# Kernel optimization log

Measured on AMD Instinct MI355X. Metric: run time of the kernel, lower is better.

## Reference

```python
import jax, jax.numpy as jnp
import numpy as np

B, N, C, H, MLP = 4, 1024, 768, 6, 2304  # num_heads = C // 128
D = C // H  # head dim = 128


def setup_inputs() -> dict:
    key = jax.random.key(0)
    ks = iter(jax.random.split(key, 64))
    def nrm(shape, s=0.02):
        return jax.random.normal(next(ks), shape, jnp.float32) * s
    inp = {}
    for nm in ("queries", "change_emb", "imageA_emb", "imageB_emb", "pe"):
        inp[nm] = jax.random.normal(next(ks), (B, N, C), jnp.float32)
    # three Attention modules: self-attn (1), change->ABC cross (2), imageAB->change cross (3)
    for i in (1, 2, 3):
        for p in ("q", "k", "v", "o"):
            inp[f"w{p}{i}"] = nrm((C, C))       # stored [in, out]; y = x @ W + b
            inp[f"b{p}{i}"] = jnp.zeros((C,), jnp.float32)
    for i in (1, 2, 3):
        inp[f"ln{i}_w"] = jnp.ones((C,), jnp.float32)
        inp[f"ln{i}_b"] = jnp.zeros((C,), jnp.float32)
    inp["mlp_w1"] = nrm((C, MLP)); inp["mlp_b1"] = jnp.zeros((MLP,), jnp.float32)
    inp["mlp_w2"] = nrm((MLP, C)); inp["mlp_b2"] = jnp.zeros((C,), jnp.float32)
    inp["flag_a"] = nrm((C,)); inp["flag_b"] = nrm((C,)); inp["flag_c"] = nrm((C,))
    return inp


def _ln(x, w, b, eps=1e-5):
    m = jnp.mean(x, -1, keepdims=True)
    v = jnp.var(x, -1, keepdims=True)
    return (x - m) * jax.lax.rsqrt(v + eps) * w + b


def _mha(q, k, v, wq, bq, wk, bk, wv, bv, wo, bo):
    b, nq, _ = q.shape
    qh = (q @ wq + bq).reshape(b, nq, H, D)
    kh = (k @ wk + bk).reshape(b, k.shape[1], H, D)
    vh = (v @ wv + bv).reshape(b, v.shape[1], H, D)
    scores = jnp.einsum('bqhd,bkhd->bhqk', qh, kh) / np.float32(np.sqrt(D))
    attn = jax.nn.softmax(scores, axis=-1)
    out = jnp.einsum('bhqk,bkhd->bqhd', attn, vh).reshape(b, nq, H * D)
    return out @ wo + bo


def reference(queries, change_emb, imageA_emb, imageB_emb, pe,
              wq1, bq1, wk1, bk1, wv1, bv1, wo1, bo1,
              wq2, bq2, wk2, bk2, wv2, bv2, wo2, bo2,
              wq3, bq3, wk3, bk3, wv3, bv3, wo3, bo3,
              ln1_w, ln1_b, ln2_w, ln2_b, ln3_w, ln3_b,
              mlp_w1, mlp_b1, mlp_w2, mlp_b2,
              flag_a, flag_b, flag_c):
    # --- self attention on change queries (skip_first_layer_add=False) ---
    q0 = queries + change_emb
    a = _mha(q0 + pe, q0 + pe, q0, wq1, bq1, wk1, bk1, wv1, bv1, wo1, bo1)
    q1 = _ln(q0 + a, ln1_w, ln1_b)
    # --- cross attention: change -> [imageA, imageB, change] ---
    qf = q1 + pe + flag_c
    k2 = jnp.concatenate((imageA_emb + pe + flag_a,
                          imageB_emb + pe + flag_b,
                          q1 + pe + flag_c), axis=1)
    v2 = jnp.concatenate((imageA_emb, imageB_emb, q1), axis=1)
    a = _mha(qf, k2, v2, wq2, bq2, wk2, bk2, wv2, bv2, wo2, bo2)
    q2 = _ln(q1 + a, ln2_w, ln2_b)
    # --- MLP (exact GELU, as nn.GELU default) ---
    mlp_out = jax.nn.gelu(q2 @ mlp_w1 + mlp_b1, approximate=False) @ mlp_w2 + mlp_b2
    q3 = _ln(q2 + mlp_out, ln3_w, ln3_b)
    change_out = q3
    # --- cross attention: [imageA; imageB] -> [image; change], batched along dim 0 ---
    qa = imageA_emb + pe + flag_a
    qb = imageB_emb + pe + flag_b
    ka = jnp.concatenate((imageA_emb + pe + flag_a, q3 + pe + flag_c), axis=1)
    kb = jnp.concatenate((imageB_emb + pe + flag_b, q3 + pe + flag_c), axis=1)
    va = jnp.concatenate((imageA_emb, q3), axis=1)
    vb = jnp.concatenate((imageB_emb, q3), axis=1)
    q = jnp.concatenate((qa, qb), axis=0)   # [2B, N, C]
    k = jnp.concatenate((ka, kb), axis=0)   # [2B, 2N, C]
    v = jnp.concatenate((va, vb), axis=0)
    a = _mha(q, k, v, wq3, bq3, wk3, bk3, wv3, bv3, wo3, bo3)
    q = q + a
    image_A_refined, image_B_refined = jnp.split(q, 2, axis=0)
    return (image_A_refined, image_B_refined, change_out)
```

## Files before the change

### kernel.cpp

```cpp
#include <hip/hip_runtime.h>
#include <hip/hip_bf16.h>
#include <math.h>

typedef short bf16x8 __attribute__((ext_vector_type(8)));
typedef float f32x4 __attribute__((ext_vector_type(4)));
using bf16_t = __hip_bfloat16;

#define DEV static __device__ __forceinline__

DEV unsigned short f2bu(float x) {
  bf16_t h = __float2bfloat16(x);
  unsigned short u;
  __builtin_memcpy(&u, &h, 2);
  return u;
}
DEV void st4(bf16_t* p, float a, float b, float c, float d) {
  ushort4 u;
  u.x = f2bu(a); u.y = f2bu(b); u.z = f2bu(c); u.w = f2bu(d);
  *reinterpret_cast<ushort4*>(p) = u;
}

DEV void async_copy16(const bf16_t* g, bf16_t* lds) {
  __builtin_amdgcn_global_load_lds(
      (const __attribute__((address_space(1))) unsigned int*)g,
      (__attribute__((address_space(3))) unsigned int*)lds, 16, 0, 0);
}

struct WPack {
  const float* s[12];
  bf16_t* d[12];
  float scale0;
};

__global__ __launch_bounds__(256) void k_wt12(WPack pk) {
  __shared__ float tile[32][33];
  int z = blockIdx.z;
  const float* W = pk.s[z];
  bf16_t* WT = pk.d[z];
  float scale = (z == 0) ? pk.scale0 : 1.0f;
  int i0 = blockIdx.x * 32;
  int o0 = blockIdx.y * 32;
  int tx = threadIdx.x & 31, ty = threadIdx.x >> 5;
  for (int r = ty; r < 32; r += 8)
    tile[r][tx] = W[(size_t)(i0 + r) * 768 + (o0 + tx)];
  __syncthreads();
  for (int r = ty; r < 32; r += 8)
    WT[(size_t)(o0 + r) * 768 + (i0 + tx)] = __float2bfloat16(tile[tx][r] * scale);
}

__global__ __launch_bounds__(256) void k_wt(const float* __restrict__ W, bf16_t* __restrict__ WT,
                                            int in_dim, int out_dim) {
  __shared__ float tile[32][33];
  int i0 = blockIdx.x * 32;
  int o0 = blockIdx.y * 32;
  int tx = threadIdx.x & 31, ty = threadIdx.x >> 5;
  for (int r = ty; r < 32; r += 8)
    tile[r][tx] = W[(size_t)(i0 + r) * out_dim + (o0 + tx)];
  __syncthreads();
  for (int r = ty; r < 32; r += 8)
    WT[(size_t)(o0 + r) * in_dim + (i0 + tx)] = __float2bfloat16(tile[tx][r]);
}

__global__ __launch_bounds__(256) void k_bqk(const float* __restrict__ bq, const float* __restrict__ bk,
                                             float* __restrict__ out, float qa) {
  int i = blockIdx.x * 256 + threadIdx.x;
  if (i < 768) out[i] = bq[i] * qa;
  else if (i < 1536) out[i] = bk[i - 768];
}

__global__ __launch_bounds__(256) void k_prep1(const float4* __restrict__ q, const float4* __restrict__ ce,
                                               const float4* __restrict__ pe,
                                               bf16_t* __restrict__ qpe_b, bf16_t* __restrict__ q0_b, int n4) {
  int i = blockIdx.x * 256 + threadIdx.x;
  if (i >= n4) return;
  float4 a = q[i], b = ce[i], p = pe[i];
  float sx = a.x + b.x, sy = a.y + b.y, sz = a.z + b.z, sw = a.w + b.w;
  st4(q0_b + 4 * (size_t)i, sx, sy, sz, sw);
  st4(qpe_b + 4 * (size_t)i, sx + p.x, sy + p.y, sz + p.z, sw + p.w);
}

__global__ __launch_bounds__(256) void k_addpe(const float* __restrict__ x, const float* __restrict__ pe,
                                               const float* __restrict__ flag, bf16_t* __restrict__ out) {
  int idx = blockIdx.x * 256 + threadIdx.x;
  int c = (idx % 192) * 4;
  size_t tok = (size_t)idx * 4;
  float4 xv = *(const float4*)(x + tok);
  float4 p = *(const float4*)(pe + tok);
  float4 f = *(const float4*)(flag + c);
  st4(out + tok, xv.x + p.x + f.x, xv.y + p.y + f.y, xv.z + p.z + f.z, xv.w + p.w + f.w);
}

__global__ __launch_bounds__(256) void k_buildqq(const float* __restrict__ imA, const float* __restrict__ imB,
                                                 const float* __restrict__ pe, const float* __restrict__ fa,
                                                 const float* __restrict__ fb, bf16_t* __restrict__ qq) {
  int idx = blockIdx.x * 256 + threadIdx.x;
  int c4 = idx % 192; int rem = idx / 192;
  int n = rem & 1023; int bb = rem >> 10;
  int b = bb & 3, isB = bb >> 2;
  int c = c4 * 4;
  size_t tok = (size_t)(b * 1024 + n) * 768 + c;
  float4 s = *(const float4*)((isB ? imB : imA) + tok);
  float4 p = *(const float4*)(pe + tok);
  float4 f = *(const float4*)((isB ? fb : fa) + c);
  st4(qq + (size_t)rem * 768 + c, s.x + p.x + f.x, s.y + p.y + f.y, s.z + p.z + f.z, s.w + p.w + f.w);
}

__global__ __launch_bounds__(256) void k_build2b(const float* __restrict__ q1,
    const float* __restrict__ imA, const float* __restrict__ imB, const float* __restrict__ pe,
    const float* __restrict__ fa, const float* __restrict__ fb, const float* __restrict__ fc,
    bf16_t* __restrict__ k2, bf16_t* __restrict__ v2, int b0) {
  int idx = blockIdx.x * 256 + threadIdx.x;
  int c4 = idx % 192; int rem = idx / 192;
  int bi = rem / 3072; int r3 = rem - bi * 3072;
  int seg = r3 >> 10; int n = r3 & 1023;
  int b = b0 + bi;
  int c = c4 * 4;
  size_t tok = (size_t)(b * 1024 + n) * 768 + c;
  float4 p = *(const float4*)(pe + tok);
  const float* srcp; const float* flg;
  if (seg == 0)      { srcp = imA + tok; flg = fa; }
  else if (seg == 1) { srcp = imB + tok; flg = fb; }
  else               { srcp = q1 + tok; flg = fc; }
  float4 s = *(const float4*)srcp;
  float4 f = *(const float4*)(flg + c);
  size_t o = (size_t)idx * 4;
  st4(v2 + o, s.x, s.y, s.z, s.w);
  st4(k2 + o, s.x + p.x + f.x, s.y + p.y + f.y, s.z + p.z + f.z, s.w + p.w + f.w);
}

__global__ __launch_bounds__(256) void k_build3b(const float* __restrict__ q3,
    const float* __restrict__ imA, const float* __restrict__ imB, const float* __restrict__ pe,
    const float* __restrict__ fa, const float* __restrict__ fb, const float* __restrict__ fc,
    bf16_t* __restrict__ k3, bf16_t* __restrict__ v3, int bb0) {
  int idx = blockIdx.x * 256 + threadIdx.x;
  int c4 = idx % 192; int rem = idx / 192;
  int bi = rem >> 11; int r2 = rem & 2047;
  int seg = r2 >> 10; int n = r2 & 1023;
  int bb = bb0 + bi;
  int b = bb & 3; int isB = bb >> 2;
  int c = c4 * 4;
  size_t tok = (size_t)(b * 1024 + n) * 768 + c;
  float4 p = *(const float4*)(pe + tok);
  const float* srcp; const float* flg;
  if (seg == 0) { srcp = (isB ? imB : imA) + tok; flg = isB ? fb : fa; }
  else          { srcp = q3 + tok; flg = fc; }
  float4 s = *(const float4*)srcp;
  float4 f = *(const float4*)(flg + c);
  size_t o = (size_t)idx * 4;
  st4(v3 + o, s.x, s.y, s.z, s.w);
  st4(k3 + o, s.x + p.x + f.x, s.y + p.y + f.y, s.z + p.z + f.z, s.w + p.w + f.w);
}

__global__ __launch_bounds__(256, 3) void k_flash(
    const bf16_t* __restrict__ Q, const bf16_t* __restrict__ K,
    const bf16_t* __restrict__ Vt, bf16_t* __restrict__ O,
    int Nk, int H, int ldq, int ldk, long qStrideB, long kStrideB, long oStrideB) {
  const int z = blockIdx.y; const int b = z / H, h = z % H;
  const bf16_t* Qb = Q + (size_t)b * qStrideB + h * 128;
  const bf16_t* Kb = K + (size_t)b * kStrideB + h * 128;
  const bf16_t* Vb = Vt + (size_t)z * 128 * (size_t)Nk;
  bf16_t* Ob = O + (size_t)b * oStrideB + h * 128;
  const int q0 = blockIdx.x * 64;
  const int tid = threadIdx.x, lane = tid & 63, w = tid >> 6;
  const int g = lane >> 4, c = lane & 15;

  __shared__ bf16_t Ks[64][136];
  __shared__ bf16_t Vs[128][72];
  __shared__ bf16_t Ps[64][72];

  bf16x8 qf[4];
#pragma unroll
  for (int kk = 0; kk < 4; kk++)
    qf[kk] = *reinterpret_cast<const bf16x8*>(
        &Qb[(size_t)(q0 + w * 16 + c) * ldq + kk * 32 + g * 8]);

  f32x4 oa[8];
  float m[4], l[4];
#pragma unroll
  for (int d = 0; d < 8; d++) { f32x4 zz = {0.f, 0.f, 0.f, 0.f}; oa[d] = zz; }
#pragma unroll
  for (int r = 0; r < 4; r++) { m[r] = -1.0e30f; l[r] = 0.f; }

  const int kr_ = tid >> 4, kc_ = (tid & 15) * 8;
  const int vr_ = tid >> 3, vc_ = (tid & 7) * 8;

  const int nt = Nk >> 6;
  for (int t = 0; t < nt; ++t) {
    const int k0 = t << 6;
#pragma unroll
    for (int p = 0; p < 4; p++)
      *reinterpret_cast<uint4*>(&Ks[p * 16 + kr_][kc_]) =
          *reinterpret_cast<const uint4*>(&Kb[(size_t)(k0 + p * 16 + kr_) * ldk + kc_]);
#pragma unroll
    for (int p = 0; p < 4; p++)
      *reinterpret_cast<uint4*>(&Vs[p * 32 + vr_][vc_]) =
          *reinterpret_cast<const uint4*>(&Vb[(size_t)(p * 32 + vr_) * Nk + k0 + vc_]);
    __syncthreads();

    f32x4 s[4];
#pragma unroll
    for (int j = 0; j < 4; j++) { f32x4 zz = {0.f, 0.f, 0.f, 0.f}; s[j] = zz; }
    __builtin_amdgcn_s_setprio(1);
#pragma unroll
    for (int kk = 0; kk < 4; kk++)
#pragma unroll
      for (int j = 0; j < 4; j++) {
        bf16x8 kf = *reinterpret_cast<const bf16x8*>(&Ks[j * 16 + c][kk * 32 + g * 8]);
        s[j] = __builtin_amdgcn_mfma_f32_16x16x32_bf16(qf[kk], kf, s[j], 0, 0, 0);
      }
    __builtin_amdgcn_s_setprio(0);

    float tl[4];
#pragma unroll
    for (int r = 0; r < 4; r++)
      tl[r] = fmaxf(fmaxf(s[0][r], s[1][r]), fmaxf(s[2][r], s[3][r]));
    float ex = fmaxf(fmaxf(tl[0] - m[0], tl[1] - m[1]), fmaxf(tl[2] - m[2], tl[3] - m[3]));
    if (__any(ex > 8.0f)) {
#pragma unroll
      for (int r = 0; r < 4; r++) {
        float tv = tl[r];
        tv = fmaxf(tv, __shfl_xor(tv, 1));
        tv = fmaxf(tv, __shfl_xor(tv, 2));
        tv = fmaxf(tv, __shfl_xor(tv, 4));
        tv = fmaxf(tv, __shfl_xor(tv, 8));
        float mn = fmaxf(m[r], tv);
        float f = exp2f(m[r] - mn);
        m[r] = mn;
        l[r] *= f;
#pragma unroll
        for (int d = 0; d < 8; d++) oa[d][r] *= f;
      }
    }
#pragma unroll
    for (int j = 0; j < 4; j++)
#pragma unroll
      for (int r = 0; r < 4; r++) {
        float p = exp2f(s[j][r] - m[r]);
        l[r] += p;
        Ps[w * 16 + g * 4 + r][j * 16 + c] = __float2bfloat16(p);
      }

    __builtin_amdgcn_s_setprio(1);
#pragma unroll
    for (int kk = 0; kk < 2; kk++) {
      bf16x8 pf = *reinterpret_cast<const bf16x8*>(&Ps[w * 16 + c][kk * 32 + g * 8]);
#pragma unroll
      for (int d = 0; d < 8; d++) {
        bf16x8 vf = *reinterpret_cast<const bf16x8*>(&Vs[d * 16 + c][kk * 32 + g * 8]);
        oa[d] = __builtin_amdgcn_mfma_f32_16x16x32_bf16(pf, vf, oa[d], 0, 0, 0);
      }
    }
    __builtin_amdgcn_s_setprio(0);
    __syncthreads();
  }

  float inv[4];
#pragma unroll
  for (int r = 0; r < 4; r++) {
    float t2 = l[r];
    t2 += __shfl_xor(t2, 1);
    t2 += __shfl_xor(t2, 2);
    t2 += __shfl_xor(t2, 4);
    t2 += __shfl_xor(t2, 8);
    inv[r] = 1.0f / t2;
  }
#pragma unroll
  for (int d = 0; d < 8; d++) {
    int col = d * 16 + c;
#pragma unroll
    for (int r = 0; r < 4; r++) {
      int row = q0 + w * 16 + g * 4 + r;
      Ob[(size_t)row * 768 + col] = __float2bfloat16(oa[d][r] * inv[r]);
    }
  }
}

__global__ __launch_bounds__(256) void k_ln(const float* __restrict__ X1, const float* __restrict__ X2,
                                            const float* __restrict__ A,
                                            const float* __restrict__ w, const float* __restrict__ bvec,
                                            float* __restrict__ outf, bf16_t* __restrict__ outb) {
  int row = blockIdx.x, tid = threadIdx.x;
  size_t base = (size_t)row * 768;
  float v0 = X1[base + tid] + A[base + tid];
  float v1 = X1[base + tid + 256] + A[base + tid + 256];
  float v2 = X1[base + tid + 512] + A[base + tid + 512];
  if (X2) {
    v0 += X2[base + tid]; v1 += X2[base + tid + 256]; v2 += X2[base + tid + 512];
  }
  float s = v0 + v1 + v2;
  for (int o = 32; o; o >>= 1) s += __shfl_xor(s, o);
  __shared__ float sm[8];
  int wv = tid >> 6, ln = tid & 63;
  if (ln == 0) sm[wv] = s;
  __syncthreads();
  s = sm[0] + sm[1] + sm[2] + sm[3];
  float mean = s * (1.0f / 768.0f);
  float d0 = v0 - mean, d1 = v1 - mean, d2 = v2 - mean;
  float ss = d0 * d0 + d1 * d1 + d2 * d2;
  for (int o = 32; o; o >>= 1) ss += __shfl_xor(ss, o);
  if (ln == 0) sm[4 + wv] = ss;
  __syncthreads();
  ss = sm[4] + sm[5] + sm[6] + sm[7];
  float rstd = rsqrtf(ss * (1.0f / 768.0f) + 1e-5f);
  float o0 = d0 * rstd * w[tid] + bvec[tid];
  float o1 = d1 * rstd * w[tid + 256] + bvec[tid + 256];
  float o2 = d2 * rstd * w[tid + 512] + bvec[tid + 512];
  outf[base + tid] = o0; outf[base + tid + 256] = o1; outf[base + tid + 512] = o2;
  if (outb) {
    outb[base + tid] = __float2bfloat16(o0);
    outb[base + tid + 256] = __float2bfloat16(o1);
    outb[base + tid + 512] = __float2bfloat16(o2);
  }
}

struct GArgs {
  const bf16_t* X; const bf16_t* Wt; const float* bias; void* Out;
  const bf16_t* resid;
  int K, ldx, ldw, ldo, vNk, mode;
  float alpha;
};

__global__ __launch_bounds__(256, 2) void k_gemmM(GArgs a0, GArgs a1, GArgs a2,
                                                  int c0, int c01, int nx0, int nx1, int nx2) {
  GArgs a; int bx, by;
  {
    int idx = blockIdx.x;
    if (idx < c0) { a = a0; bx = idx % nx0; by = idx / nx0; }
    else if (idx < c01) { idx -= c0; a = a1; bx = idx % nx1; by = idx / nx1; }
    else { idx -= c01; a = a2; bx = idx % nx2; by = idx / nx2; }
  }
  const int brow = by * 128;
  const int bcol = bx * 128;

  __shared__ bf16_t As[128 * 32];
  __shared__ bf16_t Bs[128 * 32];

  const int tid = threadIdx.x;
  const int lane = tid & 63;
  const int wave = tid >> 6;
  const int wr = wave >> 1;
  const int wc = wave & 1;

  f32x4 acc[4][4];
#pragma unroll
  for (int i = 0; i < 4; i++)
#pragma unroll
    for (int j = 0; j < 4; j++) {
      f32x4 zz = {0.f, 0.f, 0.f, 0.f};
      acc[i][j] = zz;
    }

  const int sr = lane >> 2;
  const int sc = (lane & 3) * 8;
  const int lrow = lane & 15;
  const int kch = (lane >> 4) * 8;

  const int nK = a.K >> 5;
  for (int kk = 0; kk < nK; ++kk) {
    const int k0 = kk << 5;
#pragma unroll
    for (int q = 0; q < 2; q++) {
      const int rows = wave * 32 + q * 16;
      async_copy16(a.X + (size_t)(brow + rows + sr) * a.ldx + k0 + sc, As + rows * 32);
      async_copy16(a.Wt + (size_t)(bcol + rows + sr) * a.ldw + k0 + sc, Bs + rows * 32);
    }
    __syncthreads();

    bf16x8 afr[4], bfr[4];
#pragma unroll
    for (int i = 0; i < 4; i++)
      afr[i] = *reinterpret_cast<const bf16x8*>(&As[(wr * 64 + i * 16 + lrow) * 32 + kch]);
#pragma unroll
    for (int j = 0; j < 4; j++)
      bfr[j] = *reinterpret_cast<const bf16x8*>(&Bs[(wc * 64 + j * 16 + lrow) * 32 + kch]);
#pragma unroll
    for (int i = 0; i < 4; i++)
#pragma unroll
      for (int j = 0; j < 4; j++)
        acc[i][j] = __builtin_amdgcn_mfma_f32_16x16x32_bf16(afr[i], bfr[j], acc[i][j], 0, 0, 0);
    __syncthreads();
  }

  const int lcol = lane & 15;
  const int lrow4 = (lane >> 4) * 4;

  if (a.mode == 2) {
    const int bi = brow / a.vNk;
    const int n0 = brow - bi * a.vNk;
#pragma unroll
    for (int i = 0; i < 4; i++) {
      int rloc = n0 + wr * 64 + i * 16 + lrow4;
#pragma unroll
      for (int j = 0; j < 4; j++) {
        int col = bcol + wc * 64 + j * 16 + lcol;
        int hh = col >> 7, dd = col & 127;
        float bv = a.bias[col];
        ushort4 u;
        u.x = f2bu(acc[i][j][0] + bv);
        u.y = f2bu(acc[i][j][1] + bv);
        u.z = f2bu(acc[i][j][2] + bv);
        u.w = f2bu(acc[i][j][3] + bv);
        bf16_t* dst = reinterpret_cast<bf16_t*>(a.Out) +
                      ((size_t)(bi * 6 + hh) * 128 + dd) * (size_t)a.vNk + rloc;
        *reinterpret_cast<ushort4*>(dst) = u;
      }
    }
  } else if (a.mode == 3) {
#pragma unroll
    for (int i = 0; i < 4; i++) {
      int row0 = brow + wr * 64 + i * 16 + lrow4;
#pragma unroll
      for (int j = 0; j < 4; j++) {
        int col = bcol + wc * 64 + j * 16 + lcol;
        float bv = a.bias[col];
#pragma unroll
        for (int r = 0; r < 4; r++) {
          size_t idx = (size_t)(row0 + r) * a.ldo + col;
          float rv = __bfloat162float(a.resid[(size_t)(row0 + r) * 768 + col]);
          reinterpret_cast<float*>(a.Out)[idx] = acc[i][j][r] + bv + rv;
        }
      }
    }
  } else {
#pragma unroll
    for (int i = 0; i < 4; i++) {
      int row0 = brow + wr * 64 + i * 16 + lrow4;
#pragma unroll
      for (int j = 0; j < 4; j++) {
        int col = bcol + wc * 64 + j * 16 + lcol;
        float bv = a.bias[col];
#pragma unroll
        for (int r = 0; r < 4; r++)
          reinterpret_cast<bf16_t*>(a.Out)[(size_t)(row0 + r) * a.ldo + col] =
              __float2bfloat16((acc[i][j][r] + bv) * a.alpha);
      }
    }
  }
}

static inline void gemmM3(hipStream_t st, GArgs a0, int M0, int N0,
                          GArgs a1, int M1, int N1, GArgs a2, int M2, int N2) {
  int nx0 = N0 / 128, nx1 = N1 / 128, nx2 = N2 > 0 ? N2 / 128 : 1;
  int c0 = nx0 * (M0 / 128), c1 = nx1 * (M1 / 128), c2 = nx2 * (M2 / 128);
  k_gemmM<<<dim3(c0 + c1 + c2), 256, 0, st>>>(a0, a1, a2, c0, c0 + c1, nx0, nx1, nx2);
}

template<int OUTBF, int GELU>
__global__ __launch_bounds__(256, 2) void k_gemm(
    const bf16_t* __restrict__ X, const bf16_t* __restrict__ Wt,
    const float* __restrict__ bias, void* __restrict__ Out,
    int M, int Nout, int K, int ldx, int ldw, int ldo, float alpha) {
  const int brow = blockIdx.y * 128;
  const int bcol = blockIdx.x * 128;

  __shared__ bf16_t As[128 * 32];
  __shared__ bf16_t Bs[128 * 32];

  const int tid = threadIdx.x;
  const int lane = tid & 63;
  const int wave = tid >> 6;
  const int wr = wave >> 1;
  const int wc = wave & 1;

  f32x4 acc[4][4];
#pragma unroll
  for (int i = 0; i < 4; i++)
#pragma unroll
    for (int j = 0; j < 4; j++) {
      f32x4 zz = {0.f, 0.f, 0.f, 0.f};
      acc[i][j] = zz;
    }

  const int sr = lane >> 2;
  const int sc = (lane & 3) * 8;
  const int lrow = lane & 15;
  const int kch = (lane >> 4) * 8;

  const int nK = K >> 5;
  for (int kk = 0; kk < nK; ++kk) {
    const int k0 = kk << 5;
#pragma unroll
    for (int q = 0; q < 2; q++) {
      const int rows = wave * 32 + q * 16;
      async_copy16(X + (size_t)(brow + rows + sr) * ldx + k0 + sc, As + rows * 32);
      async_copy16(Wt + (size_t)(bcol + rows + sr) * ldw + k0 + sc, Bs + rows * 32);
    }
    __syncthreads();

    bf16x8 afr[4], bfr[4];
#pragma unroll
    for (int i = 0; i < 4; i++)
      afr[i] = *reinterpret_cast<const bf16x8*>(&As[(wr * 64 + i * 16 + lrow) * 32 + kch]);
#pragma unroll
    for (int j = 0; j < 4; j++)
      bfr[j] = *reinterpret_cast<const bf16x8*>(&Bs[(wc * 64 + j * 16 + lrow) * 32 + kch]);
#pragma unroll
    for (int i = 0; i < 4; i++)
#pragma unroll
      for (int j = 0; j < 4; j++)
        acc[i][j] = __builtin_amdgcn_mfma_f32_16x16x32_bf16(afr[i], bfr[j], acc[i][j], 0, 0, 0);
    __syncthreads();
  }

  const int lcol = lane & 15;
  const int lrow4 = (lane >> 4) * 4;

#pragma unroll
  for (int i = 0; i < 4; i++) {
    int row0 = brow + wr * 64 + i * 16 + lrow4;
#pragma unroll
    for (int j = 0; j < 4; j++) {
      int col = bcol + wc * 64 + j * 16 + lcol;
      float bv = bias ? bias[col] : 0.0f;
#pragma unroll
      for (int r = 0; r < 4; r++) {
        float v = (acc[i][j][r] + bv) * alpha;
        if (GELU) v = 0.5f * v * (1.0f + erff(v * 0.70710678118f));
        size_t idx = (size_t)(row0 + r) * ldo + col;
        if (OUTBF) reinterpret_cast<bf16_t*>(Out)[idx] = __float2bfloat16(v);
        else reinterpret_cast<float*>(Out)[idx] = v;
      }
    }
  }
}

static inline void gemm(hipStream_t st, const bf16_t* X, const bf16_t* Wt, const float* bias,
                        void* out, int outBf, int gelu, int M, int N, int K,
                        int ldx, int ldw, int ldo, float alpha = 1.0f) {
  dim3 g(N / 128, M / 128), blk(256);
  if (outBf) {
    if (gelu) k_gemm<1, 1><<<g, blk, 0, st>>>(X, Wt, bias, out, M, N, K, ldx, ldw, ldo, alpha);
    else      k_gemm<1, 0><<<g, blk, 0, st>>>(X, Wt, bias, out, M, N, K, ldx, ldw, ldo, alpha);
  } else      k_gemm<0, 0><<<g, blk, 0, st>>>(X, Wt, bias, out, M, N, K, ldx, ldw, ldo, alpha);
}

extern "C" void kernel_launch(void* const* d_in, const int* in_sizes, int n_in,
                              void* d_out, int out_size, void* d_ws, size_t ws_size,
                              hipStream_t stream) {
  (void)in_sizes; (void)n_in; (void)out_size;
  constexpr int B = 4, N = 1024, C = 768, Hh = 6, MLPD = 2304;
  constexpr size_t BNC = (size_t)B * N * C;
  constexpr size_t NC  = (size_t)N * C;
  const float scale = 0.08838834764831845f;
  const float qalpha = scale * 1.4426950408889634f;

  const float* queries = (const float*)d_in[0];
  const float* change  = (const float*)d_in[1];
  const float* imA     = (const float*)d_in[2];
  const float* imB     = (const float*)d_in[3];
  const float* pe      = (const float*)d_in[4];
  const float* bq1 = (const float*)d_in[6];  const float* bk1 = (const float*)d_in[8];
  const float* bv1 = (const float*)d_in[10]; const float* bo1 = (const float*)d_in[12];
  const float* bq2 = (const float*)d_in[14]; const float* bk2 = (const float*)d_in[16];
  const float* bv2 = (const float*)d_in[18]; const float* bo2 = (const float*)d_in[20];
  const float* bq3 = (const float*)d_in[22]; const float* bk3 = (const float*)d_in[24];
  const float* bv3 = (const float*)d_in[26]; const float* bo3 = (const float*)d_in[28];
  const float* ln1w = (const float*)d_in[29]; const float* ln1b = (const float*)d_in[30];
  const float* ln2w = (const float*)d_in[31]; const float* ln2b = (const float*)d_in[32];
  const float* ln3w = (const float*)d_in[33]; const float* ln3b = (const float*)d_in[34];
  const float* mb1 = (const float*)d_in[36]; const float* mb2 = (const float*)d_in[38];
  const float* fa = (const float*)d_in[39];
  const float* fb = (const float*)d_in[40];
  const float* fc = (const float*)d_in[41];

  char* base = (char*)d_ws;
  size_t off = 0;
  auto alloc = [&](size_t bytes) -> void* {
    void* p = base + off;
    off += (bytes + 255) & ~(size_t)255;
    return p;
  };

  bf16_t* WT[14];
  const int widx[14] = {5, 7, 9, 11, 13, 15, 17, 19, 21, 23, 25, 27, 35, 37};
  const int wins[14] = {768, 768, 768, 768, 768, 768, 768, 768, 768, 768, 768, 768, 768, 2304};
  const int wout[14] = {768, 768, 768, 768, 768, 768, 768, 768, 768, 768, 768, 768, 2304, 768};
  for (int i = 0; i < 14; i++) WT[i] = (bf16_t*)alloc((size_t)wins[i] * wout[i] * 2);
  float* bqk1 = (float*)alloc(1536 * 4);
  float*  q1  = (float*)alloc(BNC * 4);
  float*  q2  = (float*)alloc(BNC * 4);
  bf16_t* q2b = (bf16_t*)alloc(BNC * 2);
  bf16_t* qq    = (bf16_t*)alloc(2 * BNC * 2);
  bf16_t* Q3h   = (bf16_t*)alloc(2 * BNC * 2);
  const size_t arena = off;

  const size_t slack = 4u << 20;
  size_t rem = (ws_size > arena + slack) ? ws_size - arena - slack : 0;
  int g2 = 4;
  while (g2 > 1 && 3 * BNC * 2 + (size_t)g2 * 4 * (3 * NC * 2) > rem) g2 >>= 1;
  int h3 = 8;
  while (h3 > 1 && BNC * 2 + (size_t)h3 * 4 * (2 * NC * 2) > rem) h3 >>= 1;

  float* dof = (float*)d_out;
  float* chg = dof + 2 * BNC;

  WPack pk;
  for (int i = 0; i < 12; i++) { pk.s[i] = (const float*)d_in[widx[i]]; pk.d[i] = WT[i]; }
  pk.scale0 = qalpha;
  k_wt12<<<dim3(24, 24, 12), 256, 0, stream>>>(pk);
  k_wt<<<dim3(24, 72), 256, 0, stream>>>((const float*)d_in[35], WT[12], 768, 2304);
  k_wt<<<dim3(72, 24), 256, 0, stream>>>((const float*)d_in[37], WT[13], 2304, 768);
  k_bqk<<<dim3(6), 256, 0, stream>>>(bq1, bk1, bqk1, qalpha);

  off = arena;
  bf16_t* qpe_b = (bf16_t*)alloc(BNC * 2);
  bf16_t* q0_b  = (bf16_t*)alloc(BNC * 2);
  bf16_t* QKh   = (bf16_t*)alloc((size_t)B * N * 1536 * 2);
  bf16_t* vT1   = (bf16_t*)alloc(BNC * 2);
  bf16_t* attC  = (bf16_t*)alloc(BNC * 2);
  float*  a1    = dof;

  k_prep1<<<dim3((int)(BNC / 4 / 256)), 256, 0, stream>>>(
      (const float4*)queries, (const float4*)change, (const float4*)pe, qpe_b, q0_b, (int)(BNC / 4));
  k_buildqq<<<dim3((int)(2 * BNC / 4 / 256)), 256, 0, stream>>>(imA, imB, pe, fa, fb, qq);
  {
    GArgs aqk = {qpe_b, WT[0], bqk1, QKh, nullptr, C, C, C, 1536, 0, 1, 1.0f};
    GArgs av  = {q0_b,  WT[2], bv1,  vT1, nullptr, C, C, C, 0,  N, 2, 1.0f};
    GArgs aq3 = {qq,    WT[8], bq3,  Q3h, nullptr, C, C, C, C,  0, 1, qalpha};
    gemmM3(stream, aqk, B * N, 1536, av, B * N, C, aq3, 2 * B * N, C);
  }
  k_flash<<<dim3(N / 64, B * Hh), 256, 0, stream>>>(QKh, QKh + 768, vT1, attC,
                                                    N, Hh, 1536, 1536,
                                                    (long)N * 1536, (long)N * 1536, (long)NC);
  gemm(stream, attC, WT[3], bo1, a1, 0, 0, B * N, C, C, C, C, C);
  k_ln<<<dim3(B * N), 256, 0, stream>>>(queries, change, a1, ln1w, ln1b, q1, (bf16_t*)nullptr);

  off = arena;
  bf16_t* qf    = (bf16_t*)alloc(BNC * 2);
  bf16_t* Q2h   = (bf16_t*)alloc(BNC * 2);
  bf16_t* attC2 = (bf16_t*)alloc(BNC * 2);
  bf16_t* k2in  = (bf16_t*)alloc((size_t)g2 * 3 * NC * 2);
  bf16_t* v2in  = (bf16_t*)alloc((size_t)g2 * 3 * NC * 2);
  bf16_t* K2h   = (bf16_t*)alloc((size_t)g2 * 3 * NC * 2);
  bf16_t* vT2   = (bf16_t*)alloc((size_t)g2 * 3 * NC * 2);
  float*  a2    = dof;

  k_addpe<<<dim3((int)(BNC / 4 / 256)), 256, 0, stream>>>(q1, pe, fc, qf);
  if (g2 == 4) {
    const int Nk = 3 * N;
    k_build2b<<<dim3((int)((size_t)4 * 3 * NC / 4 / 256)), 256, 0, stream>>>(
        q1, imA, imB, pe, fa, fb, fc, k2in, v2in, 0);
    GArgs aq = {qf,   WT[4], bq2, Q2h, nullptr, C, C, C, C, 0, 1, qalpha};
    GArgs ak = {k2in, WT[5], bk2, K2h, nullptr, C, C, C, C, 0, 1, 1.0f};
    GArgs av = {v2in, WT[6], bv2, vT2, nullptr, C, C, C, 0, Nk, 2, 1.0f};
    gemmM3(stream, aq, B * N, C, ak, 4 * Nk, C, av, 4 * Nk, C);
    k_flash<<<dim3(N / 64, 4 * Hh), 256, 0, stream>>>(Q2h, K2h, vT2, attC2, Nk, Hh, C, C,
                                                      (long)NC, (long)(3 * NC), (long)NC);
  } else {
    gemm(stream, qf, WT[4], bq2, Q2h, 1, 0, B * N, C, C, C, C, C, qalpha);
    for (int b0 = 0; b0 < B; b0 += g2) {
      const int Nk = 3 * N;
      k_build2b<<<dim3((int)((size_t)g2 * 3 * NC / 4 / 256)), 256, 0, stream>>>(
          q1, imA, imB, pe, fa, fb, fc, k2in, v2in, b0);
      GArgs ak = {k2in, WT[5], bk2, K2h, nullptr, C, C, C, C, 0, 1, 1.0f};
      GArgs av = {v2in, WT[6], bv2, vT2, nullptr, C, C, C, 0, Nk, 2, 1.0f};
      gemmM3(stream, ak, g2 * Nk, C, av, g2 * Nk, C, av, 0, 128);
      k_flash<<<dim3(N / 64, g2 * Hh), 256, 0, stream>>>(Q2h + (size_t)b0 * NC, K2h, vT2,
                                                         attC2 + (size_t)b0 * NC, Nk, Hh, C, C,
                                                         (long)NC, (long)(3 * NC), (long)NC);
    }
  }
  gemm(stream, attC2, WT[7], bo2, a2, 0, 0, B * N, C, C, C, C, C);
  k_ln<<<dim3(B * N), 256, 0, stream>>>(q1, (const float*)nullptr, a2, ln2w, ln2b, q2, q2b);

  off = arena;
  bf16_t* h1 = (bf16_t*)alloc((size_t)B * N * MLPD * 2);
  float*  a3 = dof;
  gemm(stream, q2b, WT[12], mb1, h1, 1, 1, B * N, MLPD, C, C, C, MLPD);
  gemm(stream, h1, WT[13], mb2, a3, 0, 0, B * N, C, MLPD, MLPD, MLPD, C);
  k_ln<<<dim3(B * N), 256, 0, stream>>>(q2, (const float*)nullptr, a3, ln3w, ln3b, chg, (bf16_t*)nullptr);

  off = arena;
  bf16_t* attC3 = (bf16_t*)alloc(2 * BNC * 2);
  bf16_t* k3in  = (bf16_t*)alloc((size_t)h3 * 2 * NC * 2);
  bf16_t* v3in  = (bf16_t*)alloc((size_t)h3 * 2 * NC * 2);
  bf16_t* K3h   = (bf16_t*)alloc((size_t)h3 * 2 * NC * 2);
  bf16_t* vT3   = (bf16_t*)alloc((size_t)h3 * 2 * NC * 2);

  for (int bb0 = 0; bb0 < 2 * B; bb0 += h3) {
    const int Nk = 2 * N;
    k_build3b<<<dim3((int)((size_t)h3 * 2 * NC / 4 / 256)), 256, 0, stream>>>(
        chg, imA, imB, pe, fa, fb, fc, k3in, v3in, bb0);
    GArgs ak = {k3in, WT[9],  bk3, K3h, nullptr, C, C, C, C, 0, 1, 1.0f};
    GArgs av = {v3in, WT[10], bv3, vT3, nullptr, C, C, C, 0, Nk, 2, 1.0f};
    gemmM3(stream, ak, h3 * Nk, C, av, h3 * Nk, C, av, 0, 128);
    k_flash<<<dim3(N / 64, h3 * Hh), 256, 0, stream>>>(Q3h + (size_t)bb0 * NC, K3h, vT3,
                                                       attC3 + (size_t)bb0 * NC, Nk, Hh, C, C,
                                                       (long)NC, (long)(2 * NC), (long)NC);
  }
  {
    GArgs ao = {attC3, WT[11], bo3, dof, qq, C, C, C, C, 0, 3, 1.0f};
    gemmM3(stream, ao, 2 * B * N, C, ao, 0, 128, ao, 0, 128);
  }
}
```

Baseline: 692.9 us.

## Prefetch next K/V tile into registers while computing current tile in flash attention

The flash-attention loop now loads the next 64-key K and V tile from global memory into registers before computing on the current LDS tile. After the compute it writes those registers to shared memory between two barriers, so global latency overlaps with MFMA work. The launch bound drops from 3 to 2 blocks per SIMD so the 8 extra uint4 registers per thread fit. This trades occupancy for software prefetching.

```diff
diff --git a/kernel.cpp b/kernel.cpp
--- a/kernel.cpp
+++ b/kernel.cpp
@@ -151,7 +151,7 @@
   st4(k3 + o, s.x + p.x + f.x, s.y + p.y + f.y, s.z + p.z + f.z, s.w + p.w + f.w);
 }
 
-__global__ __launch_bounds__(256, 3) void k_flash(
+__global__ __launch_bounds__(256, 2) void k_flash(
     const bf16_t* __restrict__ Q, const bf16_t* __restrict__ K,
     const bf16_t* __restrict__ Vt, bf16_t* __restrict__ O,
     int Nk, int H, int ldq, int ldk, long qStrideB, long kStrideB, long oStrideB) {
@@ -184,19 +184,27 @@
   const int kr_ = tid >> 4, kc_ = (tid & 15) * 8;
   const int vr_ = tid >> 3, vc_ = (tid & 7) * 8;
 
-  const int nt = Nk >> 6;
-  for (int t = 0; t < nt; ++t) {
-    const int k0 = t << 6;
-#pragma unroll
-    for (int p = 0; p < 4; p++)
-      *reinterpret_cast<uint4*>(&Ks[p * 16 + kr_][kc_]) =
-          *reinterpret_cast<const uint4*>(&Kb[(size_t)(k0 + p * 16 + kr_) * ldk + kc_]);
-#pragma unroll
-    for (int p = 0; p < 4; p++)
-      *reinterpret_cast<uint4*>(&Vs[p * 32 + vr_][vc_]) =
-          *reinterpret_cast<const uint4*>(&Vb[(size_t)(p * 32 + vr_) * Nk + k0 + vc_]);
-    __syncthreads();
-
+  {
+    uint4 ka0 = *reinterpret_cast<const uint4*>(&Kb[(size_t)(kr_) * ldk + kc_]);
+    uint4 ka1 = *reinterpret_cast<const uint4*>(&Kb[(size_t)(16 + kr_) * ldk + kc_]);
+    uint4 ka2 = *reinterpret_cast<const uint4*>(&Kb[(size_t)(32 + kr_) * ldk + kc_]);
+    uint4 ka3 = *reinterpret_cast<const uint4*>(&Kb[(size_t)(48 + kr_) * ldk + kc_]);
+    uint4 va0 = *reinterpret_cast<const uint4*>(&Vb[(size_t)(vr_) * Nk + vc_]);
+    uint4 va1 = *reinterpret_cast<const uint4*>(&Vb[(size_t)(32 + vr_) * Nk + vc_]);
+    uint4 va2 = *reinterpret_cast<const uint4*>(&Vb[(size_t)(64 + vr_) * Nk + vc_]);
+    uint4 va3 = *reinterpret_cast<const uint4*>(&Vb[(size_t)(96 + vr_) * Nk + vc_]);
+    *reinterpret_cast<uint4*>(&Ks[kr_][kc_]) = ka0;
+    *reinterpret_cast<uint4*>(&Ks[16 + kr_][kc_]) = ka1;
+    *reinterpret_cast<uint4*>(&Ks[32 + kr_][kc_]) = ka2;
+    *reinterpret_cast<uint4*>(&Ks[48 + kr_][kc_]) = ka3;
+    *reinterpret_cast<uint4*>(&Vs[vr_][vc_]) = va0;
+    *reinterpret_cast<uint4*>(&Vs[32 + vr_][vc_]) = va1;
+    *reinterpret_cast<uint4*>(&Vs[64 + vr_][vc_]) = va2;
+    *reinterpret_cast<uint4*>(&Vs[96 + vr_][vc_]) = va3;
+  }
+  __syncthreads();
+
+  auto compute = [&]() {
     f32x4 s[4];
 #pragma unroll
     for (int j = 0; j < 4; j++) { f32x4 zz = {0.f, 0.f, 0.f, 0.f}; s[j] = zz; }
@@ -251,8 +259,34 @@
       }
     }
     __builtin_amdgcn_s_setprio(0);
+  };
+
+  const int nt = Nk >> 6;
+  for (int t = 0; t < nt - 1; ++t) {
+    const int kn = (t + 1) << 6;
+    uint4 ka0 = *reinterpret_cast<const uint4*>(&Kb[(size_t)(kn + kr_) * ldk + kc_]);
+    uint4 ka1 = *reinterpret_cast<const uint4*>(&Kb[(size_t)(kn + 16 + kr_) * ldk + kc_]);
+    uint4 ka2 = *reinterpret_cast<const uint4*>(&Kb[(size_t)(kn + 32 + kr_) * ldk + kc_]);
+    uint4 ka3 = *reinterpret_cast<const uint4*>(&Kb[(size_t)(kn + 48 + kr_) * ldk + kc_]);
+    uint4 va0 = *reinterpret_cast<const uint4*>(&Vb[(size_t)(vr_) * Nk + kn + vc_]);
+    uint4 va1 = *reinterpret_cast<const uint4*>(&Vb[(size_t)(32 + vr_) * Nk + kn + vc_]);
+    uint4 va2 = *reinterpret_cast<const uint4*>(&Vb[(size_t)(64 + vr_) * Nk + kn + vc_]);
+    uint4 va3 = *reinterpret_cast<const uint4*>(&Vb[(size_t)(96 + vr_) * Nk + kn + vc_]);
+
+    compute();
+
     __syncthreads();
-  }
+    *reinterpret_cast<uint4*>(&Ks[kr_][kc_]) = ka0;
+    *reinterpret_cast<uint4*>(&Ks[16 + kr_][kc_]) = ka1;
+    *reinterpret_cast<uint4*>(&Ks[32 + kr_][kc_]) = ka2;
+    *reinterpret_cast<uint4*>(&Ks[48 + kr_][kc_]) = ka3;
+    *reinterpret_cast<uint4*>(&Vs[vr_][vc_]) = va0;
+    *reinterpret_cast<uint4*>(&Vs[32 + vr_][vc_]) = va1;
+    *reinterpret_cast<uint4*>(&Vs[64 + vr_][vc_]) = va2;
+    *reinterpret_cast<uint4*>(&Vs[96 + vr_][vc_]) = va3;
+    __syncthreads();
+  }
+  compute();
 
   float inv[4];
 #pragma unroll
```

New measurement: 702.5 us. About the same (+1.4%).
